# Performance work log

Hardware: AMD Instinct MI355X
Metric: run time of the kernel (lower is better)

The kernel has to match this reference:

```python
import jax, jax.numpy as jnp
import numpy as np

H = 128  # hidden_dim
COORD_CLAMP = 100.0


def _glorot(key, shape):
    fan_in, fan_out = shape[0], shape[1]
    lim = float(np.sqrt(6.0 / (fan_in + fan_out)))
    return jax.random.uniform(key, shape, jnp.float32, -lim, lim)


def setup_inputs() -> dict:
    key = jax.random.key(0)
    ks = jax.random.split(key, 20)
    B, N = 2, 512
    inp = {
        "h": jax.random.normal(ks[0], (B, N, H), jnp.float32),
        "pos": jax.random.normal(ks[1], (B, N, 3), jnp.float32),
        "vel": jax.random.normal(ks[2], (B, N, 3), jnp.float32),
        # edge_mlp: Linear(2H+2 -> H), SiLU, Linear(H -> H), SiLU
        "We1": _glorot(ks[3], (2 * H + 2, H)), "be1": jnp.zeros((H,), jnp.float32),
        "We2": _glorot(ks[4], (H, H)), "be2": jnp.zeros((H,), jnp.float32),
        # attention_mlp: Linear(H -> 1), Sigmoid
        "Wa": _glorot(ks[5], (H, 1)), "ba": jnp.zeros((1,), jnp.float32),
        # pos_mlp: Linear(H -> H), SiLU, Linear(H -> 1, no bias)
        "Wp1": _glorot(ks[6], (H, H)), "bp1": jnp.zeros((H,), jnp.float32),
        "Wp2": _glorot(ks[7], (H, 1)),
        # vel_mlp: Linear(H -> H), SiLU, Linear(H -> 1, no bias)
        "Wv1": _glorot(ks[8], (H, H)), "bv1": jnp.zeros((H,), jnp.float32),
        "Wv2": _glorot(ks[9], (H, 1)),
        # node_mlp: Linear(2H -> H), SiLU, Linear(H -> H)
        "Wn1": _glorot(ks[10], (2 * H, H)), "bn1": jnp.zeros((H,), jnp.float32),
        "Wn2": _glorot(ks[11], (H, H)), "bn2": jnp.zeros((H,), jnp.float32),
    }
    return inp


def reference(h, pos, vel, We1, be1, We2, be2, Wa, ba,
              Wp1, bp1, Wp2, Wv1, bv1, Wv2, Wn1, bn1, Wn2, bn2):
    B, N, _ = pos.shape
    # pairwise diffs: [B, N, N, 3]
    pos_diff = pos[:, :, None, :] - pos[:, None, :, :]
    vel_diff = vel[:, :, None, :] - vel[:, None, :, :]
    pos_dist_sq = jnp.sum(pos_diff ** 2, axis=-1, keepdims=True)  # [B,N,N,1]
    vel_dist_sq = jnp.sum(vel_diff ** 2, axis=-1, keepdims=True)
    h_i = jnp.broadcast_to(h[:, :, None, :], (B, N, N, H))
    h_j = jnp.broadcast_to(h[:, None, :, :], (B, N, N, H))
    edge_input = jnp.concatenate([h_i, h_j, pos_dist_sq, vel_dist_sq], axis=-1)  # [B,N,N,2H+2]
    # edge MLP
    m = jax.nn.silu(jnp.einsum('bijc,ch->bijh', edge_input, We1) + be1)
    m_ij = jax.nn.silu(jnp.einsum('bijh,hk->bijk', m, We2) + be2)
    # attention gate
    att = jax.nn.sigmoid(jnp.einsum('bijh,ho->bijo', m_ij, Wa) + ba)  # [B,N,N,1]
    m_ij = m_ij * att
    # tanh-weighted coordinate/velocity updates
    pos_w = jnp.tanh(jnp.einsum('bijh,ho->bijo', jax.nn.silu(jnp.einsum('bijh,hk->bijk', m_ij, Wp1) + bp1), Wp2))
    vel_w = jnp.tanh(jnp.einsum('bijh,ho->bijo', jax.nn.silu(jnp.einsum('bijh,hk->bijk', m_ij, Wv1) + bv1), Wv2))
    denom = jnp.float32(max(N - 1, 1))
    pos_update = jnp.sum(pos_diff * pos_w, axis=2) / denom  # [B,N,3]
    vel_update = jnp.sum(vel_diff * vel_w, axis=2) / denom
    pos_out = jnp.clip(pos + pos_update, -COORD_CLAMP, COORD_CLAMP)
    vel_out = jnp.clip(vel + vel_update, -COORD_CLAMP, COORD_CLAMP)
    # node update
    m_agg = jnp.sum(m_ij, axis=2)  # [B,N,H]
    node_input = jnp.concatenate([h, m_agg], axis=-1)  # [B,N,2H]
    h_out = jax.nn.silu(jnp.einsum('bnc,ch->bnh', node_input, Wn1) + bn1)
    h_out = jnp.einsum('bnh,hk->bnk', h_out, Wn2) + bn2
    h_out = h + h_out  # residual
    return (h_out, pos_out, vel_out)
```

## Files before the change

### kernel.cpp

```cpp
#include <hip/hip_runtime.h>
#include <hip/hip_bf16.h>

#define Hd 128
#define Nn 512
#define TJ 32
#define LSTRIDE 136

typedef __bf16 bf16x8 __attribute__((ext_vector_type(8)));
typedef __bf16 bf16x4 __attribute__((ext_vector_type(4)));
typedef float  floatx4 __attribute__((ext_vector_type(4)));

__device__ __forceinline__ float frcp(float x){ return __builtin_amdgcn_rcpf(x); }
__device__ __forceinline__ float fsilu(float x){ return x * frcp(1.f + __expf(-x)); }
__device__ __forceinline__ float fsigm(float x){ return frcp(1.f + __expf(-x)); }
__device__ __forceinline__ float ftanh(float x){ return 1.f - 2.f * frcp(__expf(2.f*x) + 1.f); }
__device__ __forceinline__ float rfl(float x){
  return __int_as_float(__builtin_amdgcn_readfirstlane(__float_as_int(x)));
}

__global__ __launch_bounds__(256) void prep(const float* __restrict__ h,
                                            const float* __restrict__ We1,
                                            const float* __restrict__ be1,
                                            const float* __restrict__ We2,
                                            const float* __restrict__ Wp1,
                                            const float* __restrict__ Wv1,
                                            float* __restrict__ A,
                                            float* __restrict__ Bm,
                                            __bf16* __restrict__ dst,
                                            float* __restrict__ zbase){
  if (blockIdx.x < 256){
    const int r0 = blockIdx.x * 4;
    const int k = threadIdx.x & 127, ch = threadIdx.x >> 7;
    __shared__ float hL[4][Hd];
    __shared__ float pa[2][4][Hd], pb[2][4][Hd];
    for (int idx = threadIdx.x; idx < 4*Hd; idx += 256)
      hL[idx >> 7][idx & 127] = h[r0*Hd + idx];
    __syncthreads();
    float a[4] = {0.f,0.f,0.f,0.f}, bb[4] = {0.f,0.f,0.f,0.f};
    const int cbase = ch*64;
    #pragma unroll 4
    for (int cc = 0; cc < 64; ++cc){
      const int c = cbase + cc;
      const float wa = We1[c*Hd + k];
      const float wb = We1[(c + Hd)*Hd + k];
      #pragma unroll
      for (int rr = 0; rr < 4; ++rr){
        a[rr]  += hL[rr][c] * wa;
        bb[rr] += hL[rr][c] * wb;
      }
    }
    #pragma unroll
    for (int rr = 0; rr < 4; ++rr){ pa[ch][rr][k] = a[rr]; pb[ch][rr][k] = bb[rr]; }
    __syncthreads();
    if (threadIdx.x < Hd){
      const float be = be1[k];
      #pragma unroll
      for (int rr = 0; rr < 4; ++rr){
        A[(r0+rr)*Hd + k]  = pa[0][rr][k] + pa[1][rr][k] + be;
        Bm[(r0+rr)*Hd + k] = pb[0][rr][k] + pb[1][rr][k];
      }
    }
  } else if (blockIdx.x < 280){
    const int blk = blockIdx.x - 256;
    const int which = blk >> 3, m = blk & 7;
    const float* src = (which == 0) ? We2 : (which == 1 ? Wp1 : Wv1);
    __bf16* d = dst + which * (Hd*Hd);
    #pragma unroll
    for (int it = 0; it < 8; ++it){
      const int sidx = m*2048 + it*256 + threadIdx.x;
      const int kk = sidx >> 7, cc = sidx & 127;
      const int s = kk >> 5, j = kk & 7;
      const int lane = ((kk >> 3) & 3)*16 + (cc & 15);
      const int n = cc >> 4;
      d[n*2048 + s*512 + lane*8 + j] = (__bf16)src[sidx];
    }
  } else {
    const int t0 = (blockIdx.x - 280)*256 + threadIdx.x;
    for (int idx = t0; idx < 137216; idx += 2048) zbase[idx] = 0.f;
  }
}

__device__ __forceinline__ void gemm_kloopT(const __bf16* __restrict__ buf,
                                            const bf16x8* __restrict__ Ws,
                                            int w, int lane, int q, int l15,
                                            floatx4 acc[2][2]){
  const floatx4 zero = {0.f, 0.f, 0.f, 0.f};
  #pragma unroll
  for (int m = 0; m < 2; ++m){ acc[m][0] = zero; acc[m][1] = zero; }
  #pragma unroll
  for (int s = 0; s < 4; ++s){
    bf16x8 bf[2];
    #pragma unroll
    for (int n = 0; n < 2; ++n)
      bf[n] = *(const bf16x8*)&buf[(16*n + l15)*LSTRIDE + s*32 + q*8];
    const bf16x8 a0 = Ws[((2*w + 0)*4 + s)*64 + lane];
    const bf16x8 a1 = Ws[((2*w + 1)*4 + s)*64 + lane];
    #pragma unroll
    for (int n = 0; n < 2; ++n){
      acc[0][n] = __builtin_amdgcn_mfma_f32_16x16x32_bf16(a0, bf[n], acc[0][n], 0, 0, 0);
      acc[1][n] = __builtin_amdgcn_mfma_f32_16x16x32_bf16(a1, bf[n], acc[1][n], 0, 0, 0);
    }
  }
}

__device__ __forceinline__ void wdotT(floatx4 acc[2][2], float att0, float att1,
                                      const float* __restrict__ biasL,
                                      const float* __restrict__ w2L,
                                      int w, int lane, int q, int l15,
                                      float (*part)[TJ]){
  const int fb0 = 32*w + 4*q, fb1 = fb0 + 16;
  const floatx4 bb0 = *(const floatx4*)&biasL[fb0];
  const floatx4 bb1 = *(const floatx4*)&biasL[fb1];
  const floatx4 w0  = *(const floatx4*)&w2L[fb0];
  const floatx4 w1  = *(const floatx4*)&w2L[fb1];
  float p0 = 0.f, p1 = 0.f;
  #pragma unroll
  for (int r = 0; r < 4; ++r){
    p0 += fsilu(fmaf(att0, acc[0][0][r], bb0[r])) * w0[r];
    p0 += fsilu(fmaf(att0, acc[1][0][r], bb1[r])) * w1[r];
    p1 += fsilu(fmaf(att1, acc[0][1][r], bb0[r])) * w0[r];
    p1 += fsilu(fmaf(att1, acc[1][1][r], bb1[r])) * w1[r];
  }
  p0 += __shfl_xor(p0, 16, 64); p0 += __shfl_xor(p0, 32, 64);
  p1 += __shfl_xor(p1, 16, 64); p1 += __shfl_xor(p1, 32, 64);
  if (lane < 16){
    part[w][l15]      = p0;
    part[w][16 + l15] = p1;
  }
}

__global__ __launch_bounds__(256) void egnn_main(
    const float* __restrict__ pos, const float* __restrict__ vel,
    const float* __restrict__ We1, const float* __restrict__ be2,
    const float* __restrict__ Wa,  const float* __restrict__ ba,
    const float* __restrict__ bp1, const float* __restrict__ Wp2,
    const float* __restrict__ bv1, const float* __restrict__ Wv2,
    const float* __restrict__ A,   const float* __restrict__ Bm,
    const __bf16* __restrict__ Wsw,
    float* __restrict__ magg, float* __restrict__ posu, float* __restrict__ velu){

  const int t    = threadIdx.x;
  const int w    = t >> 6;
  const int lane = t & 63;
  const int q    = lane >> 4;
  const int l15  = lane & 15;
  const int node = blockIdx.x >> 1;
  const int half = blockIdx.x & 1;
  const int b    = node >> 9;

  __shared__ float AiL[Hd], wpL[Hd], wvL[Hd];
  __shared__ float be2L[Hd], bp1L[Hd], bv1L[Hd], WaL[Hd], Wp2L[Hd], Wv2L[Hd];
  __shared__ __align__(16) __bf16 bufm [TJ*LSTRIDE];
  __shared__ __align__(16) __bf16 bufij[TJ*LSTRIDE];
  __shared__ float partAtt[4][TJ], partP[4][TJ], partV[4][TJ];
  __shared__ float attL[TJ];

  if (t < Hd){
    AiL[t]  = A[node*Hd + t];
    wpL[t]  = We1[256*Hd + t];
    wvL[t]  = We1[257*Hd + t];
    be2L[t] = be2[t]; bp1L[t] = bp1[t]; bv1L[t] = bv1[t];
    WaL[t]  = Wa[t];  Wp2L[t] = Wp2[t]; Wv2L[t] = Wv2[t];
  }
  const float baV = ba[0];
  const float* pi = &pos[(size_t)node*3];
  const float* vi = &vel[(size_t)node*3];
  const float px = rfl(pi[0]), py = rfl(pi[1]), pz = rfl(pi[2]);
  const float ux = rfl(vi[0]), uy = rfl(vi[1]), uz = rfl(vi[2]);
  __syncthreads();

  const bf16x8* We2s = (const bf16x8*)(Wsw);
  const bf16x8* Wp1s = (const bf16x8*)(Wsw + Hd*Hd);
  const bf16x8* Wv1s = (const bf16x8*)(Wsw + 2*Hd*Hd);

  float accR[8];
  #pragma unroll
  for (int e = 0; e < 8; ++e) accR[e] = 0.f;

  for (int jt = 0; jt < (Nn/2)/TJ; ++jt){
    const int j0 = half*(Nn/2) + jt * TJ;

    {
      const int g  = t & 15;
      const int j2 = t >> 4;
      const floatx4 a0 = *(const floatx4*)&AiL[g*8];
      const floatx4 a1 = *(const floatx4*)&AiL[g*8 + 4];
      const floatx4 p0 = *(const floatx4*)&wpL[g*8];
      const floatx4 p1 = *(const floatx4*)&wpL[g*8 + 4];
      const floatx4 v0 = *(const floatx4*)&wvL[g*8];
      const floatx4 v1 = *(const floatx4*)&wvL[g*8 + 4];
      #pragma unroll
      for (int rr = 0; rr < 2; ++rr){
        const int j = j2 + rr*16;
        const int jg = j0 + j;
        const float* pj = &pos[(size_t)(b*Nn + jg)*3];
        const float* vj = &vel[(size_t)(b*Nn + jg)*3];
        const float dx = px - pj[0], dy = py - pj[1], dz = pz - pj[2];
        const float dp = dx*dx + dy*dy + dz*dz;
        const float ex = ux - vj[0], ey = uy - vj[1], ez = uz - vj[2];
        const float dv = ex*ex + ey*ey + ez*ez;
        const floatx4* Bp4 = (const floatx4*)&Bm[((size_t)(b*Nn + jg))*Hd + g*8];
        const floatx4 b0 = Bp4[0], b1 = Bp4[1];
        union { bf16x8 v; __hip_bfloat162 h2[4]; } o;
        float x[8];
        #pragma unroll
        for (int e = 0; e < 4; ++e){
          x[e]   = fsilu(a0[e] + b0[e] + dp*p0[e] + dv*v0[e]);
          x[4+e] = fsilu(a1[e] + b1[e] + dp*p1[e] + dv*v1[e]);
        }
        o.h2[0] = __float22bfloat162_rn(make_float2(x[0], x[1]));
        o.h2[1] = __float22bfloat162_rn(make_float2(x[2], x[3]));
        o.h2[2] = __float22bfloat162_rn(make_float2(x[4], x[5]));
        o.h2[3] = __float22bfloat162_rn(make_float2(x[6], x[7]));
        *(bf16x8*)&bufm[j*LSTRIDE + g*8] = o.v;
      }
    }
    __syncthreads();

    {
      floatx4 acc[2][2];
      gemm_kloopT(bufm, We2s, w, lane, q, l15, acc);
      const int fb0 = 32*w + 4*q, fb1 = fb0 + 16;
      const floatx4 be0 = *(const floatx4*)&be2L[fb0];
      const floatx4 be1 = *(const floatx4*)&be2L[fb1];
      const floatx4 wa0 = *(const floatx4*)&WaL[fb0];
      const floatx4 wa1 = *(const floatx4*)&WaL[fb1];
      float aw[2];
      #pragma unroll
      for (int n = 0; n < 2; ++n){
        const int j = 16*n + l15;
        float s0[4], s1[4];
        #pragma unroll
        for (int r = 0; r < 4; ++r){
          s0[r] = fsilu(acc[0][n][r] + be0[r]);
          s1[r] = fsilu(acc[1][n][r] + be1[r]);
        }
        aw[n] = s0[0]*wa0[0] + s0[1]*wa0[1] + s0[2]*wa0[2] + s0[3]*wa0[3]
              + s1[0]*wa1[0] + s1[1]*wa1[1] + s1[2]*wa1[2] + s1[3]*wa1[3];
        union { bf16x4 v; __hip_bfloat162 h2[2]; } p0k, p1k;
        p0k.h2[0] = __float22bfloat162_rn(make_float2(s0[0], s0[1]));
        p0k.h2[1] = __float22bfloat162_rn(make_float2(s0[2], s0[3]));
        p1k.h2[0] = __float22bfloat162_rn(make_float2(s1[0], s1[1]));
        p1k.h2[1] = __float22bfloat162_rn(make_float2(s1[2], s1[3]));
        *(bf16x4*)&bufij[j*LSTRIDE + fb0] = p0k.v;
        *(bf16x4*)&bufij[j*LSTRIDE + fb1] = p1k.v;
      }
      aw[0] += __shfl_xor(aw[0], 16, 64); aw[0] += __shfl_xor(aw[0], 32, 64);
      aw[1] += __shfl_xor(aw[1], 16, 64); aw[1] += __shfl_xor(aw[1], 32, 64);
      if (lane < 16){
        partAtt[w][l15]      = aw[0];
        partAtt[w][16 + l15] = aw[1];
      }
    }
    __syncthreads();

    {
      const float att0 = fsigm(partAtt[0][l15] + partAtt[1][l15] +
                               partAtt[2][l15] + partAtt[3][l15] + baV);
      const float att1 = fsigm(partAtt[0][16+l15] + partAtt[1][16+l15] +
                               partAtt[2][16+l15] + partAtt[3][16+l15] + baV);
      if (w == 0 && lane < 16){ attL[l15] = att0; attL[16 + l15] = att1; }
      floatx4 acc[2][2];
      gemm_kloopT(bufij, Wp1s, w, lane, q, l15, acc);
      wdotT(acc, att0, att1, bp1L, Wp2L, w, lane, q, l15, partP);
      gemm_kloopT(bufij, Wv1s, w, lane, q, l15, acc);
      wdotT(acc, att0, att1, bv1L, Wv2L, w, lane, q, l15, partV);
    }
    __syncthreads();

    if (w == 0){
      if (lane < TJ){
        const int jg = j0 + lane;
        const float* pj = &pos[(size_t)(b*Nn + jg)*3];
        const float s4 = partP[0][lane] + partP[1][lane] + partP[2][lane] + partP[3][lane];
        const float pw = ftanh(s4);
        accR[0] += (px - pj[0]) * pw;
        accR[1] += (py - pj[1]) * pw;
        accR[2] += (pz - pj[2]) * pw;
      }
    } else if (w == 1){
      if (lane < TJ){
        const int jg = j0 + lane;
        const float* vj = &vel[(size_t)(b*Nn + jg)*3];
        const float s4 = partV[0][lane] + partV[1][lane] + partV[2][lane] + partV[3][lane];
        const float vw = ftanh(s4);
        accR[0] += (ux - vj[0]) * vw;
        accR[1] += (uy - vj[1]) * vw;
        accR[2] += (uz - vj[2]) * vw;
      }
    } else {
      const int sg   = (w - 2)*8 + (lane & 7);
      const int jsub = lane >> 3;
      #pragma unroll
      for (int jj = 0; jj < 4; ++jj){
        const int j = jj*8 + jsub;
        const float aj = attL[j];
        const bf16x8 v = *(const bf16x8*)&bufij[j*LSTRIDE + sg*8];
        #pragma unroll
        for (int e = 0; e < 8; ++e) accR[e] += aj * (float)v[e];
      }
    }
  }

  if (w == 0 || w == 1){
    float v0 = accR[0], v1 = accR[1], v2 = accR[2];
    #pragma unroll
    for (int off = 1; off < 64; off <<= 1){
      v0 += __shfl_xor(v0, off, 64);
      v1 += __shfl_xor(v1, off, 64);
      v2 += __shfl_xor(v2, off, 64);
    }
    if (lane == 0){
      float* dst = (w == 0) ? &posu[node*3] : &velu[node*3];
      atomicAdd(&dst[0], v0);
      atomicAdd(&dst[1], v1);
      atomicAdd(&dst[2], v2);
    }
  } else {
    const int sg = (w - 2)*8 + (lane & 7);
    #pragma unroll
    for (int off = 8; off < 64; off <<= 1){
      #pragma unroll
      for (int e = 0; e < 8; ++e) accR[e] += __shfl_xor(accR[e], off, 64);
    }
    if ((lane >> 3) == 0){
      #pragma unroll
      for (int e = 0; e < 8; ++e)
        atomicAdd(&magg[node*Hd + sg*8 + e], accR[e]);
    }
  }
}

__global__ __launch_bounds__(256) void egnn_final(
    const float* __restrict__ h, const float* __restrict__ pos, const float* __restrict__ vel,
    const float* __restrict__ Wn1, const float* __restrict__ bn1,
    const float* __restrict__ Wn2, const float* __restrict__ bn2,
    const float* __restrict__ magg, const float* __restrict__ posu,
    const float* __restrict__ velu, float* __restrict__ out){
  const int row = blockIdx.x;
  const int t = threadIdx.x;
  const int k = t & 127, ch = t >> 7;
  __shared__ float ni[2*Hd];
  __shared__ float p1[2][Hd], t1[Hd];
  ni[t] = (t < Hd) ? h[row*Hd + t] : magg[row*Hd + (t - Hd)];
  __syncthreads();
  {
    float a0=0.f,a1=0.f,a2=0.f,a3=0.f;
    const int cb = ch*Hd;
    #pragma unroll 8
    for (int cc = 0; cc < Hd; cc += 4){
      a0 += ni[cb+cc+0] * Wn1[(cb+cc+0)*Hd + k];
      a1 += ni[cb+cc+1] * Wn1[(cb+cc+1)*Hd + k];
      a2 += ni[cb+cc+2] * Wn1[(cb+cc+2)*Hd + k];
      a3 += ni[cb+cc+3] * Wn1[(cb+cc+3)*Hd + k];
    }
    p1[ch][k] = (a0+a1)+(a2+a3);
  }
  __syncthreads();
  if (t < Hd) t1[t] = fsilu(p1[0][t] + p1[1][t] + bn1[t]);
  __syncthreads();
  {
    float a0=0.f,a1=0.f,a2=0.f,a3=0.f;
    const int cb = ch*64;
    #pragma unroll 8
    for (int cc = 0; cc < 64; cc += 4){
      a0 += t1[cb+cc+0] * Wn2[(cb+cc+0)*Hd + k];
      a1 += t1[cb+cc+1] * Wn2[(cb+cc+1)*Hd + k];
      a2 += t1[cb+cc+2] * Wn2[(cb+cc+2)*Hd + k];
      a3 += t1[cb+cc+3] * Wn2[(cb+cc+3)*Hd + k];
    }
    p1[ch][k] = (a0+a1)+(a2+a3);
  }
  __syncthreads();
  if (t < Hd){
    out[row*Hd + t] = ni[t] + p1[0][t] + p1[1][t] + bn2[t];
  } else if (t < Hd + 3){
    const int d = t - Hd;
    const float v = pos[row*3 + d] + posu[row*3 + d] * (1.f/511.f);
    out[2*Nn*Hd + row*3 + d] = fminf(fmaxf(v, -100.f), 100.f);
  } else if (t < Hd + 6){
    const int d = t - Hd - 3;
    const float v = vel[row*3 + d] + velu[row*3 + d] * (1.f/511.f);
    out[2*Nn*Hd + 2*Nn*3 + row*3 + d] = fminf(fmaxf(v, -100.f), 100.f);
  }
}

extern "C" void kernel_launch(void* const* d_in, const int* in_sizes, int n_in,
                              void* d_out, int out_size, void* d_ws, size_t ws_size,
                              hipStream_t stream){
  const float* h   = (const float*)d_in[0];
  const float* pos = (const float*)d_in[1];
  const float* vel = (const float*)d_in[2];
  const float* We1 = (const float*)d_in[3];
  const float* be1 = (const float*)d_in[4];
  const float* We2 = (const float*)d_in[5];
  const float* be2 = (const float*)d_in[6];
  const float* Wa  = (const float*)d_in[7];
  const float* ba  = (const float*)d_in[8];
  const float* Wp1 = (const float*)d_in[9];
  const float* bp1 = (const float*)d_in[10];
  const float* Wp2 = (const float*)d_in[11];
  const float* Wv1 = (const float*)d_in[12];
  const float* bv1 = (const float*)d_in[13];
  const float* Wv2 = (const float*)d_in[14];
  const float* Wn1 = (const float*)d_in[15];
  const float* bn1 = (const float*)d_in[16];
  const float* Wn2 = (const float*)d_in[17];
  const float* bn2 = (const float*)d_in[18];

  float* ws = (float*)d_ws;
  float*  A    = ws;
  float*  Bmm  = ws + 131072;
  float*  magg = ws + 262144;
  float*  posu = ws + 393216;
  float*  velu = ws + 396288;
  __bf16* Wsw  = (__bf16*)(ws + 399360);

  prep      <<<dim3(288),  dim3(256), 0, stream>>>(h, We1, be1, We2, Wp1, Wv1,
                                                   A, Bmm, Wsw, magg);
  egnn_main <<<dim3(2048), dim3(256), 0, stream>>>(pos, vel, We1, be2, Wa, ba, bp1, Wp2,
                                                   bv1, Wv2, A, Bmm, Wsw, magg, posu, velu);
  egnn_final<<<dim3(1024), dim3(256), 0, stream>>>(h, pos, vel, Wn1, bn1, Wn2, bn2,
                                                   magg, posu, velu, (float*)d_out);
}
```

Baseline: 233.4 us.

## Give each wave its own 32-edge tile end-to-end, removing block barriers

Each wavefront now processes a private slab of 32 neighbor nodes across all 128 features: it builds the first-layer activations directly in registers as MFMA operands, then runs the We2, Wp1 and Wv1 GEMMs and the attention and head reductions without any cross-wave shared-memory exchange. This removes the per-tile __syncthreads barriers, the bufm staging buffer and the partial-sum arrays. The partial sums are double-counted across the q lane groups, so pos/vel atomics are scaled by 0.25 to compensate. In exchange, every wave streams the full 128x128 weight matrices per tile, which is four times the weight loads of the old split, and each thread holds 64 accumulator registers.

```diff
diff --git a/kernel.cpp b/kernel.cpp
--- a/kernel.cpp
+++ b/kernel.cpp
@@ -3,7 +3,6 @@
 
 #define Hd 128
 #define Nn 512
-#define TJ 32
 #define LSTRIDE 136
 
 typedef __bf16 bf16x8 __attribute__((ext_vector_type(8)));
@@ -80,53 +79,45 @@
   }
 }
 
-__device__ __forceinline__ void gemm_kloopT(const __bf16* __restrict__ buf,
-                                            const bf16x8* __restrict__ Ws,
-                                            int w, int lane, int q, int l15,
-                                            floatx4 acc[2][2]){
-  const floatx4 zero = {0.f, 0.f, 0.f, 0.f};
-  #pragma unroll
-  for (int m = 0; m < 2; ++m){ acc[m][0] = zero; acc[m][1] = zero; }
+__device__ __forceinline__ void gemm_w(const bf16x8* __restrict__ Ws,
+                                       const __bf16* __restrict__ myBuf,
+                                       int lane, int q, int l15,
+                                       floatx4 acc[8][2]){
+  const floatx4 fzero = {0.f,0.f,0.f,0.f};
+  #pragma unroll
+  for (int fm = 0; fm < 8; ++fm){ acc[fm][0] = fzero; acc[fm][1] = fzero; }
   #pragma unroll
   for (int s = 0; s < 4; ++s){
-    bf16x8 bf[2];
-    #pragma unroll
-    for (int n = 0; n < 2; ++n)
-      bf[n] = *(const bf16x8*)&buf[(16*n + l15)*LSTRIDE + s*32 + q*8];
-    const bf16x8 a0 = Ws[((2*w + 0)*4 + s)*64 + lane];
-    const bf16x8 a1 = Ws[((2*w + 1)*4 + s)*64 + lane];
-    #pragma unroll
-    for (int n = 0; n < 2; ++n){
-      acc[0][n] = __builtin_amdgcn_mfma_f32_16x16x32_bf16(a0, bf[n], acc[0][n], 0, 0, 0);
-      acc[1][n] = __builtin_amdgcn_mfma_f32_16x16x32_bf16(a1, bf[n], acc[1][n], 0, 0, 0);
-    }
-  }
-}
-
-__device__ __forceinline__ void wdotT(floatx4 acc[2][2], float att0, float att1,
-                                      const float* __restrict__ biasL,
-                                      const float* __restrict__ w2L,
-                                      int w, int lane, int q, int l15,
-                                      float (*part)[TJ]){
-  const int fb0 = 32*w + 4*q, fb1 = fb0 + 16;
-  const floatx4 bb0 = *(const floatx4*)&biasL[fb0];
-  const floatx4 bb1 = *(const floatx4*)&biasL[fb1];
-  const floatx4 w0  = *(const floatx4*)&w2L[fb0];
-  const floatx4 w1  = *(const floatx4*)&w2L[fb1];
+    const int fo = s*32 + q*8;
+    const bf16x8 b0 = *(const bf16x8*)&myBuf[l15*LSTRIDE + fo];
+    const bf16x8 b1 = *(const bf16x8*)&myBuf[(16 + l15)*LSTRIDE + fo];
+    #pragma unroll
+    for (int fm = 0; fm < 8; ++fm){
+      const bf16x8 a = Ws[(fm*4 + s)*64 + lane];
+      acc[fm][0] = __builtin_amdgcn_mfma_f32_16x16x32_bf16(a, b0, acc[fm][0], 0, 0, 0);
+      acc[fm][1] = __builtin_amdgcn_mfma_f32_16x16x32_bf16(a, b1, acc[fm][1], 0, 0, 0);
+    }
+  }
+}
+
+__device__ __forceinline__ float2 head_dot(floatx4 acc[8][2], float att0, float att1,
+                                           const float* __restrict__ biasL,
+                                           const float* __restrict__ w2L, int q){
   float p0 = 0.f, p1 = 0.f;
   #pragma unroll
-  for (int r = 0; r < 4; ++r){
-    p0 += fsilu(fmaf(att0, acc[0][0][r], bb0[r])) * w0[r];
-    p0 += fsilu(fmaf(att0, acc[1][0][r], bb1[r])) * w1[r];
-    p1 += fsilu(fmaf(att1, acc[0][1][r], bb0[r])) * w0[r];
-    p1 += fsilu(fmaf(att1, acc[1][1][r], bb1[r])) * w1[r];
+  for (int fm = 0; fm < 8; ++fm){
+    const int fb = fm*16 + q*4;
+    const floatx4 bb = *(const floatx4*)&biasL[fb];
+    const floatx4 w2 = *(const floatx4*)&w2L[fb];
+    #pragma unroll
+    for (int r = 0; r < 4; ++r){
+      p0 += fsilu(fmaf(att0, acc[fm][0][r], bb[r])) * w2[r];
+      p1 += fsilu(fmaf(att1, acc[fm][1][r], bb[r])) * w2[r];
+    }
   }
   p0 += __shfl_xor(p0, 16, 64); p0 += __shfl_xor(p0, 32, 64);
   p1 += __shfl_xor(p1, 16, 64); p1 += __shfl_xor(p1, 32, 64);
-  if (lane < 16){
-    part[w][l15]      = p0;
-    part[w][16 + l15] = p1;
-  }
+  return make_float2(p0, p1);
 }
 
 __global__ __launch_bounds__(256) void egnn_main(
@@ -150,10 +141,8 @@
 
   __shared__ float AiL[Hd], wpL[Hd], wvL[Hd];
   __shared__ float be2L[Hd], bp1L[Hd], bv1L[Hd], WaL[Hd], Wp2L[Hd], Wv2L[Hd];
-  __shared__ __align__(16) __bf16 bufm [TJ*LSTRIDE];
-  __shared__ __align__(16) __bf16 bufij[TJ*LSTRIDE];
-  __shared__ float partAtt[4][TJ], partP[4][TJ], partV[4][TJ];
-  __shared__ float attL[TJ];
+  __shared__ __align__(16) __bf16 bufij[4*32*LSTRIDE];
+  __shared__ float attL[128];
 
   if (t < Hd){
     AiL[t]  = A[node*Hd + t];
@@ -172,162 +161,156 @@
   const bf16x8* We2s = (const bf16x8*)(Wsw);
   const bf16x8* Wp1s = (const bf16x8*)(Wsw + Hd*Hd);
   const bf16x8* Wv1s = (const bf16x8*)(Wsw + 2*Hd*Hd);
-
-  float accR[8];
-  #pragma unroll
-  for (int e = 0; e < 8; ++e) accR[e] = 0.f;
-
-  for (int jt = 0; jt < (Nn/2)/TJ; ++jt){
-    const int j0 = half*(Nn/2) + jt * TJ;
-
+  __bf16* myBuf = &bufij[w*32*LSTRIDE];
+  float*  myAtt = &attL[w*32];
+
+  float accP0=0.f, accP1=0.f, accP2=0.f, accV0=0.f, accV1=0.f, accV2=0.f;
+  float acc8[8];
+  #pragma unroll
+  for (int e = 0; e < 8; ++e) acc8[e] = 0.f;
+
+  for (int jt = 0; jt < 2; ++jt){
+    const int jb = half*(Nn/2) + jt*128 + w*32;
+    const size_t row0 = (size_t)(b*Nn + jb + l15);
+    const size_t row1 = row0 + 16;
+
+    float dp[2], dv[2];
     {
-      const int g  = t & 15;
-      const int j2 = t >> 4;
-      const floatx4 a0 = *(const floatx4*)&AiL[g*8];
-      const floatx4 a1 = *(const floatx4*)&AiL[g*8 + 4];
-      const floatx4 p0 = *(const floatx4*)&wpL[g*8];
-      const floatx4 p1 = *(const floatx4*)&wpL[g*8 + 4];
-      const floatx4 v0 = *(const floatx4*)&wvL[g*8];
-      const floatx4 v1 = *(const floatx4*)&wvL[g*8 + 4];
-      #pragma unroll
-      for (int rr = 0; rr < 2; ++rr){
-        const int j = j2 + rr*16;
-        const int jg = j0 + j;
-        const float* pj = &pos[(size_t)(b*Nn + jg)*3];
-        const float* vj = &vel[(size_t)(b*Nn + jg)*3];
-        const float dx = px - pj[0], dy = py - pj[1], dz = pz - pj[2];
-        const float dp = dx*dx + dy*dy + dz*dz;
-        const float ex = ux - vj[0], ey = uy - vj[1], ez = uz - vj[2];
-        const float dv = ex*ex + ey*ey + ez*ez;
-        const floatx4* Bp4 = (const floatx4*)&Bm[((size_t)(b*Nn + jg))*Hd + g*8];
-        const floatx4 b0 = Bp4[0], b1 = Bp4[1];
-        union { bf16x8 v; __hip_bfloat162 h2[4]; } o;
+      const float* pj0 = &pos[row0*3]; const float* vj0 = &vel[row0*3];
+      const float* pj1 = &pos[row1*3]; const float* vj1 = &vel[row1*3];
+      float dx = px - pj0[0], dy = py - pj0[1], dz = pz - pj0[2];
+      dp[0] = dx*dx + dy*dy + dz*dz;
+      dx = px - pj1[0]; dy = py - pj1[1]; dz = pz - pj1[2];
+      dp[1] = dx*dx + dy*dy + dz*dz;
+      float ex = ux - vj0[0], ey = uy - vj0[1], ez = uz - vj0[2];
+      dv[0] = ex*ex + ey*ey + ez*ez;
+      ex = ux - vj1[0]; ey = uy - vj1[1]; ez = uz - vj1[2];
+      dv[1] = ex*ex + ey*ey + ez*ez;
+    }
+
+    floatx4 acc[8][2];
+    const floatx4 fzero = {0.f,0.f,0.f,0.f};
+    #pragma unroll
+    for (int fm = 0; fm < 8; ++fm){ acc[fm][0] = fzero; acc[fm][1] = fzero; }
+
+    #pragma unroll
+    for (int s = 0; s < 4; ++s){
+      const int fo = s*32 + q*8;
+      const floatx4 A0 = *(const floatx4*)&AiL[fo], A1 = *(const floatx4*)&AiL[fo+4];
+      const floatx4 P0 = *(const floatx4*)&wpL[fo], P1 = *(const floatx4*)&wpL[fo+4];
+      const floatx4 V0 = *(const floatx4*)&wvL[fo], V1 = *(const floatx4*)&wvL[fo+4];
+      bf16x8 mf[2];
+      #pragma unroll
+      for (int n = 0; n < 2; ++n){
+        const floatx4* Bp = (const floatx4*)&Bm[(n ? row1 : row0)*Hd + fo];
+        const floatx4 b0 = Bp[0], b1 = Bp[1];
         float x[8];
         #pragma unroll
         for (int e = 0; e < 4; ++e){
-          x[e]   = fsilu(a0[e] + b0[e] + dp*p0[e] + dv*v0[e]);
-          x[4+e] = fsilu(a1[e] + b1[e] + dp*p1[e] + dv*v1[e]);
+          x[e]   = fsilu(A0[e] + b0[e] + dp[n]*P0[e] + dv[n]*V0[e]);
+          x[4+e] = fsilu(A1[e] + b1[e] + dp[n]*P1[e] + dv[n]*V1[e]);
         }
+        union { bf16x8 v; __hip_bfloat162 h2[4]; } o;
         o.h2[0] = __float22bfloat162_rn(make_float2(x[0], x[1]));
         o.h2[1] = __float22bfloat162_rn(make_float2(x[2], x[3]));
         o.h2[2] = __float22bfloat162_rn(make_float2(x[4], x[5]));
         o.h2[3] = __float22bfloat162_rn(make_float2(x[6], x[7]));
-        *(bf16x8*)&bufm[j*LSTRIDE + g*8] = o.v;
-      }
-    }
-    __syncthreads();
-
+        mf[n] = o.v;
+      }
+      #pragma unroll
+      for (int fm = 0; fm < 8; ++fm){
+        const bf16x8 a = We2s[(fm*4 + s)*64 + lane];
+        acc[fm][0] = __builtin_amdgcn_mfma_f32_16x16x32_bf16(a, mf[0], acc[fm][0], 0, 0, 0);
+        acc[fm][1] = __builtin_amdgcn_mfma_f32_16x16x32_bf16(a, mf[1], acc[fm][1], 0, 0, 0);
+      }
+    }
+
+    float aw0 = 0.f, aw1 = 0.f;
+    #pragma unroll
+    for (int fm = 0; fm < 8; ++fm){
+      const int fb = fm*16 + q*4;
+      const floatx4 be = *(const floatx4*)&be2L[fb];
+      const floatx4 wa = *(const floatx4*)&WaL[fb];
+      float s0[4], s1[4];
+      #pragma unroll
+      for (int r = 0; r < 4; ++r){
+        s0[r] = fsilu(acc[fm][0][r] + be[r]);
+        s1[r] = fsilu(acc[fm][1][r] + be[r]);
+        aw0 += s0[r]*wa[r];
+        aw1 += s1[r]*wa[r];
+      }
+      union { bf16x4 v; __hip_bfloat162 h2[2]; } k0, k1;
+      k0.h2[0] = __float22bfloat162_rn(make_float2(s0[0], s0[1]));
+      k0.h2[1] = __float22bfloat162_rn(make_float2(s0[2], s0[3]));
+      k1.h2[0] = __float22bfloat162_rn(make_float2(s1[0], s1[1]));
+      k1.h2[1] = __float22bfloat162_rn(make_float2(s1[2], s1[3]));
+      *(bf16x4*)&myBuf[l15*LSTRIDE + fb]        = k0.v;
+      *(bf16x4*)&myBuf[(16 + l15)*LSTRIDE + fb] = k1.v;
+    }
+    aw0 += __shfl_xor(aw0, 16, 64); aw0 += __shfl_xor(aw0, 32, 64);
+    aw1 += __shfl_xor(aw1, 16, 64); aw1 += __shfl_xor(aw1, 32, 64);
+    const float att0 = fsigm(aw0 + baV);
+    const float att1 = fsigm(aw1 + baV);
+    if (lane < 16){ myAtt[l15] = att0; myAtt[16 + l15] = att1; }
+
+    gemm_w(Wp1s, myBuf, lane, q, l15, acc);
     {
-      floatx4 acc[2][2];
-      gemm_kloopT(bufm, We2s, w, lane, q, l15, acc);
-      const int fb0 = 32*w + 4*q, fb1 = fb0 + 16;
-      const floatx4 be0 = *(const floatx4*)&be2L[fb0];
-      const floatx4 be1 = *(const floatx4*)&be2L[fb1];
-      const floatx4 wa0 = *(const floatx4*)&WaL[fb0];
-      const floatx4 wa1 = *(const floatx4*)&WaL[fb1];
-      float aw[2];
-      #pragma unroll
-      for (int n = 0; n < 2; ++n){
-        const int j = 16*n + l15;
-        float s0[4], s1[4];
+      const float2 pp = head_dot(acc, att0, att1, bp1L, Wp2L, q);
+      const float pw0 = ftanh(pp.x), pw1 = ftanh(pp.y);
+      const float* pj0 = &pos[row0*3];
+      const float* pj1 = &pos[row1*3];
+      accP0 += (px - pj0[0])*pw0 + (px - pj1[0])*pw1;
+      accP1 += (py - pj0[1])*pw0 + (py - pj1[1])*pw1;
+      accP2 += (pz - pj0[2])*pw0 + (pz - pj1[2])*pw1;
+    }
+
+    gemm_w(Wv1s, myBuf, lane, q, l15, acc);
+    {
+      const float2 vv = head_dot(acc, att0, att1, bv1L, Wv2L, q);
+      const float vw0 = ftanh(vv.x), vw1 = ftanh(vv.y);
+      const float* vj0 = &vel[row0*3];
+      const float* vj1 = &vel[row1*3];
+      accV0 += (ux - vj0[0])*vw0 + (ux - vj1[0])*vw1;
+      accV1 += (uy - vj0[1])*vw0 + (uy - vj1[1])*vw1;
+      accV2 += (uz - vj0[2])*vw0 + (uz - vj1[2])*vw1;
+    }
+
+    {
+      const int fg = lane & 15, jr = lane >> 4;
+      #pragma unroll
+      for (int k = 0; k < 8; ++k){
+        const int jl = jr + 4*k;
+        const float aj = myAtt[jl];
+        const bf16x8 v = *(const bf16x8*)&myBuf[jl*LSTRIDE + fg*8];
         #pragma unroll
-        for (int r = 0; r < 4; ++r){
-          s0[r] = fsilu(acc[0][n][r] + be0[r]);
-          s1[r] = fsilu(acc[1][n][r] + be1[r]);
-        }
-        aw[n] = s0[0]*wa0[0] + s0[1]*wa0[1] + s0[2]*wa0[2] + s0[3]*wa0[3]
-              + s1[0]*wa1[0] + s1[1]*wa1[1] + s1[2]*wa1[2] + s1[3]*wa1[3];
-        union { bf16x4 v; __hip_bfloat162 h2[2]; } p0k, p1k;
-        p0k.h2[0] = __float22bfloat162_rn(make_float2(s0[0], s0[1]));
-        p0k.h2[1] = __float22bfloat162_rn(make_float2(s0[2], s0[3]));
-        p1k.h2[0] = __float22bfloat162_rn(make_float2(s1[0], s1[1]));
-        p1k.h2[1] = __float22bfloat162_rn(make_float2(s1[2], s1[3]));
-        *(bf16x4*)&bufij[j*LSTRIDE + fb0] = p0k.v;
-        *(bf16x4*)&bufij[j*LSTRIDE + fb1] = p1k.v;
-      }
-      aw[0] += __shfl_xor(aw[0], 16, 64); aw[0] += __shfl_xor(aw[0], 32, 64);
-      aw[1] += __shfl_xor(aw[1], 16, 64); aw[1] += __shfl_xor(aw[1], 32, 64);
-      if (lane < 16){
-        partAtt[w][l15]      = aw[0];
-        partAtt[w][16 + l15] = aw[1];
-      }
-    }
-    __syncthreads();
-
-    {
-      const float att0 = fsigm(partAtt[0][l15] + partAtt[1][l15] +
-                               partAtt[2][l15] + partAtt[3][l15] + baV);
-      const float att1 = fsigm(partAtt[0][16+l15] + partAtt[1][16+l15] +
-                               partAtt[2][16+l15] + partAtt[3][16+l15] + baV);
-      if (w == 0 && lane < 16){ attL[l15] = att0; attL[16 + l15] = att1; }
-      floatx4 acc[2][2];
-      gemm_kloopT(bufij, Wp1s, w, lane, q, l15, acc);
-      wdotT(acc, att0, att1, bp1L, Wp2L, w, lane, q, l15, partP);
-      gemm_kloopT(bufij, Wv1s, w, lane, q, l15, acc);
-      wdotT(acc, att0, att1, bv1L, Wv2L, w, lane, q, l15, partV);
-    }
-    __syncthreads();
-
-    if (w == 0){
-      if (lane < TJ){
-        const int jg = j0 + lane;
-        const float* pj = &pos[(size_t)(b*Nn + jg)*3];
-        const float s4 = partP[0][lane] + partP[1][lane] + partP[2][lane] + partP[3][lane];
-        const float pw = ftanh(s4);
-        accR[0] += (px - pj[0]) * pw;
-        accR[1] += (py - pj[1]) * pw;
-        accR[2] += (pz - pj[2]) * pw;
-      }
-    } else if (w == 1){
-      if (lane < TJ){
-        const int jg = j0 + lane;
-        const float* vj = &vel[(size_t)(b*Nn + jg)*3];
-        const float s4 = partV[0][lane] + partV[1][lane] + partV[2][lane] + partV[3][lane];
-        const float vw = ftanh(s4);
-        accR[0] += (ux - vj[0]) * vw;
-        accR[1] += (uy - vj[1]) * vw;
-        accR[2] += (uz - vj[2]) * vw;
-      }
-    } else {
-      const int sg   = (w - 2)*8 + (lane & 7);
-      const int jsub = lane >> 3;
-      #pragma unroll
-      for (int jj = 0; jj < 4; ++jj){
-        const int j = jj*8 + jsub;
-        const float aj = attL[j];
-        const bf16x8 v = *(const bf16x8*)&bufij[j*LSTRIDE + sg*8];
-        #pragma unroll
-        for (int e = 0; e < 8; ++e) accR[e] += aj * (float)v[e];
-      }
-    }
-  }
-
-  if (w == 0 || w == 1){
-    float v0 = accR[0], v1 = accR[1], v2 = accR[2];
-    #pragma unroll
-    for (int off = 1; off < 64; off <<= 1){
-      v0 += __shfl_xor(v0, off, 64);
-      v1 += __shfl_xor(v1, off, 64);
-      v2 += __shfl_xor(v2, off, 64);
-    }
-    if (lane == 0){
-      float* dst = (w == 0) ? &posu[node*3] : &velu[node*3];
-      atomicAdd(&dst[0], v0);
-      atomicAdd(&dst[1], v1);
-      atomicAdd(&dst[2], v2);
-    }
-  } else {
-    const int sg = (w - 2)*8 + (lane & 7);
-    #pragma unroll
-    for (int off = 8; off < 64; off <<= 1){
-      #pragma unroll
-      for (int e = 0; e < 8; ++e) accR[e] += __shfl_xor(accR[e], off, 64);
-    }
-    if ((lane >> 3) == 0){
-      #pragma unroll
-      for (int e = 0; e < 8; ++e)
-        atomicAdd(&magg[node*Hd + sg*8 + e], accR[e]);
-    }
+        for (int e = 0; e < 8; ++e) acc8[e] += aj * (float)v[e];
+      }
+    }
+  }
+
+  float r6[6] = {accP0, accP1, accP2, accV0, accV1, accV2};
+  #pragma unroll
+  for (int off = 1; off < 64; off <<= 1){
+    #pragma unroll
+    for (int e = 0; e < 6; ++e) r6[e] += __shfl_xor(r6[e], off, 64);
+  }
+  if (lane == 0){
+    atomicAdd(&posu[node*3+0], r6[0]*0.25f);
+    atomicAdd(&posu[node*3+1], r6[1]*0.25f);
+    atomicAdd(&posu[node*3+2], r6[2]*0.25f);
+    atomicAdd(&velu[node*3+0], r6[3]*0.25f);
+    atomicAdd(&velu[node*3+1], r6[4]*0.25f);
+    atomicAdd(&velu[node*3+2], r6[5]*0.25f);
+  }
+  #pragma unroll
+  for (int e = 0; e < 8; ++e){
+    acc8[e] += __shfl_xor(acc8[e], 16, 64);
+    acc8[e] += __shfl_xor(acc8[e], 32, 64);
+  }
+  if (lane < 16){
+    #pragma unroll
+    for (int e = 0; e < 8; ++e)
+      atomicAdd(&magg[node*Hd + lane*8 + e], acc8[e]);
   }
 }
 
```

Measured after the change: 856.6 us. 3.67x slower.
